# Optimization experiments

Hardware: AMD Instinct MI355X
Metric: run time of the kernel (lower is better)

Reference implementation:

```python
import jax, jax.numpy as jnp
import numpy as np

B, T, H, C, R = 8, 8192, 128, 128, 128  # batch, points, hidden, c_dim, plane reso
EPS = 1e-3  # 10e-4 in original
PLANE_COLS = ((0, 2), (0, 1), (1, 2))  # xz, xy, yz


def _normalize_coordinate(p, cols):
    # normalize_coordinate with padding=0.0: p in [-0.5,0.5] -> [0,1), clipped
    xy = p[..., jnp.array(cols)] / (1.0 + 0.0 + EPS) + 0.5
    return jnp.clip(xy, 0.0, 1.0 - EPS)


def _coordinate2index(xy):
    g = jnp.floor(xy * R).astype(jnp.int32)  # [B,T,2]
    return g[..., 0] + R * g[..., 1]  # [B,T]


def _resblock(x, w0, b0, w1, b1, ws):
    # ResnetBlockFC: fc_1(relu(fc_0(relu(x)))) + shortcut(x)
    net = jax.nn.relu(x) @ w0 + b0
    dx = jax.nn.relu(net) @ w1 + b1
    return x @ ws + dx


def _pool_local(c, idx_list):
    # c: [B,T,F]; scatter_max into R*R bins per plane, gather back, sum over planes
    def one(cb, ib):  # cb [T,F], ib [T]
        out = jnp.full((R * R, cb.shape[-1]), -jnp.inf, cb.dtype).at[ib].max(cb)
        out = jnp.where(jnp.isinf(out), jnp.zeros_like(out), out)  # empty bins -> 0
        return out[ib]  # gather-broadcast back to points
    pooled = jnp.zeros_like(c)
    for idx in idx_list:
        pooled = pooled + jax.vmap(one)(c, idx)
    return pooled


def _plane_features(cfeat, idx):
    # scatter_mean of [B,T,C] into [B, C, R, R]
    def one(cb, ib):  # cb [T,C], ib [T]
        sums = jnp.zeros((R * R, cb.shape[-1]), cb.dtype).at[ib].add(cb)
        cnt = jnp.zeros((R * R,), cb.dtype).at[ib].add(1.0)
        return sums / jnp.clip(cnt, 1.0, None)[:, None]
    m = jax.vmap(one)(cfeat, idx)  # [B, R*R, C]
    return m.transpose(0, 2, 1).reshape(cfeat.shape[0], cfeat.shape[-1], R, R)


def _forward(p, p2, wp, bp, wp2, bp2,
             blk_w0, blk_b0, blk_w1, blk_b1, blk_ws,
             blkc_w0, blkc_b0, blkc_w1, blkc_b1, blkc_ws,
             fc_c_w, fc_c_b, fc_cc_w, fc_cc_b):
    idx_list = [_coordinate2index(_normalize_coordinate(p, cols)) for cols in PLANE_COLS]

    # feat_pos (PointNetPlusPlusAttnFusion) surrogate: per-point projections + additive fusion
    net = p @ wp + bp                  # [B,T,2H] geometry stream
    net_corr = net + (p2 @ wp2 + bp2)  # [B,T,2H] fused articulation stream

    net = _resblock(net, blk_w0[0], blk_b0[0], blk_w1[0], blk_b1[0], blk_ws[0])
    for i in range(1, blk_w0.shape[0]):
        pooled = _pool_local(net, idx_list)
        net = _resblock(jnp.concatenate([net, pooled], axis=-1),
                        blk_w0[i], blk_b0[i], blk_w1[i], blk_b1[i], blk_ws[i])
    c = net @ fc_c_w + fc_c_b  # [B,T,C]

    net_corr = _resblock(net_corr, blkc_w0[0], blkc_b0[0], blkc_w1[0], blkc_b1[0], blkc_ws[0])
    for i in range(1, blkc_w0.shape[0]):
        pooled = _pool_local(net_corr, idx_list)
        net_corr = _resblock(jnp.concatenate([net_corr, pooled], axis=-1),
                             blkc_w0[i], blkc_b0[i], blkc_w1[i], blkc_b1[i], blkc_ws[i])
    c_corr = net_corr @ fc_cc_w + fc_cc_b  # [B,T,C]

    planes = [_plane_features(c, idx) for idx in idx_list]
    planes += [_plane_features(c_corr, idx) for idx in idx_list]
    # order: geo_xz, geo_xy, geo_yz, corr_xz, corr_xy, corr_yz
    return jnp.stack(planes)  # [6, B, C, R, R]


def setup_inputs() -> dict:
    key = jax.random.key(0)
    ks = jax.random.split(key, 24)
    s = 0.05
    def n(i, shape):
        return jax.random.normal(ks[i], shape, jnp.float32) * s
    NB = 5
    return {
        "p": jax.random.uniform(ks[0], (B, T, 3), jnp.float32, -0.5, 0.5),
        "p2": jax.random.uniform(ks[1], (B, T, 3), jnp.float32, -0.5, 0.5),
        "wp": n(2, (3, 2 * H)), "bp": jnp.zeros((2 * H,), jnp.float32),
        "wp2": n(3, (3, 2 * H)), "bp2": jnp.zeros((2 * H,), jnp.float32),
        "blk_w0": n(4, (NB, 2 * H, H)), "blk_b0": jnp.zeros((NB, H), jnp.float32),
        "blk_w1": n(5, (NB, H, H)), "blk_b1": jnp.zeros((NB, H), jnp.float32),
        "blk_ws": n(6, (NB, 2 * H, H)),
        "blkc_w0": n(7, (NB, 2 * H, H)), "blkc_b0": jnp.zeros((NB, H), jnp.float32),
        "blkc_w1": n(8, (NB, H, H)), "blkc_b1": jnp.zeros((NB, H), jnp.float32),
        "blkc_ws": n(9, (NB, 2 * H, H)),
        "fc_c_w": n(10, (H, C)), "fc_c_b": jnp.zeros((C,), jnp.float32),
        "fc_cc_w": n(11, (H, C)), "fc_cc_b": jnp.zeros((C,), jnp.float32),
    }


def reference(p, p2, wp, bp, wp2, bp2,
              blk_w0, blk_b0, blk_w1, blk_b1, blk_ws,
              blkc_w0, blkc_b0, blkc_w1, blkc_b1, blkc_ws,
              fc_c_w, fc_c_b, fc_cc_w, fc_cc_b):
    return _forward(p, p2, wp, bp, wp2, bp2,
                    blk_w0, blk_b0, blk_w1, blk_b1, blk_ws,
                    blkc_w0, blkc_b0, blkc_w1, blkc_b1, blkc_ws,
                    fc_c_w, fc_c_b, fc_cc_w, fc_cc_b)
```

## Files before the change

### kernel.cpp

```cpp
#include <hip/hip_runtime.h>
#include <cstdint>
#include <cstddef>

#define Bn 8
#define Tn 8192
#define BT (Bn*Tn)
#define Hn 128
#define RRn 16384

typedef unsigned short u16;
typedef __attribute__((ext_vector_type(8))) short s8v;
typedef __attribute__((ext_vector_type(4))) float f4v;

#define SSTR ((size_t)BT*128)

__device__ __forceinline__ u16 f2bf(float f) {
  unsigned u = __float_as_uint(f);
  unsigned r = (u + 0x7FFF + ((u >> 16) & 1)) >> 16;
  return (u16)r;
}
__device__ __forceinline__ unsigned pack2(float a, float b) {
  return (unsigned)f2bf(a) | ((unsigned)f2bf(b) << 16);
}

__device__ __forceinline__ s8v relu8(s8v a) {
  union { s8v s; unsigned u[4]; } x; x.s = a;
#pragma unroll
  for (int k = 0; k < 4; ++k) {
    unsigned m = ((x.u[k] & 0x80008000u) >> 15) * 0xFFFFu;
    x.u[k] &= ~m;
  }
  return x.s;
}

__device__ __forceinline__ void upk(unsigned u, float& lo, float& hi) {
  lo = __uint_as_float(u << 16);
  hi = __uint_as_float(u & 0xFFFF0000u);
}

__global__ void k_idx(const float* __restrict__ p, int* __restrict__ idx,
                      int* __restrict__ cnt32) {
  int i = blockIdx.x*256 + threadIdx.x;
  if (i >= BT) return;
  int b = i >> 13;
  float v0 = p[i*3+0], v1 = p[i*3+1], v2 = p[i*3+2];
  float v[3] = {v0, v1, v2};
  const int A0[3] = {0,0,1};
  const int A1[3] = {2,1,2};
#pragma unroll
  for (int pl = 0; pl < 3; ++pl) {
    float a = v[A0[pl]] / 1.001f + 0.5f;
    float bq = v[A1[pl]] / 1.001f + 0.5f;
    a = fminf(fmaxf(a, 0.0f), 0.999f);
    bq = fminf(fmaxf(bq, 0.0f), 0.999f);
    int ga = (int)floorf(a * 128.0f);
    int gb = (int)floorf(bq * 128.0f);
    int bin = ga + 128*gb;
    idx[pl*BT + i] = bin;
    atomicAdd(&cnt32[(pl*Bn + b)*RRn + bin], 1);
  }
}

__global__ void k_scan(const int* __restrict__ cnt32, int* __restrict__ starts,
                       int* __restrict__ cursor) {
  int seg = blockIdx.x;
  const int* c = cnt32 + seg*RRn;
  int* st = starts + seg*RRn;
  int* cu = cursor + seg*RRn;
  int t = threadIdx.x;
  __shared__ int part[256];
  int base = t*64;
  int sum = 0;
#pragma unroll 8
  for (int j = 0; j < 64; ++j) sum += c[base+j];
  part[t] = sum; __syncthreads();
  for (int ofs = 1; ofs < 256; ofs <<= 1) {
    int v = (t >= ofs) ? part[t-ofs] : 0;
    __syncthreads();
    part[t] += v;
    __syncthreads();
  }
  int run = (t ? part[t-1] : 0) + seg*Tn;
#pragma unroll 8
  for (int j = 0; j < 64; ++j) { st[base+j] = run; cu[base+j] = run; run += c[base+j]; }
}

__global__ void k_fill(const int* __restrict__ idx, int* __restrict__ cursor,
                       int* __restrict__ sorted) {
  int g = blockIdx.x*256 + threadIdx.x;
  if (g >= 3*BT) return;
  int pl = g >> 16, i = g & (BT-1);
  int b = i >> 13;
  int pos = atomicAdd(&cursor[(pl*Bn + b)*RRn + idx[g]], 1);
  sorted[pos] = i;
}

__global__ void k_prep(const float* __restrict__ bw0, const float* __restrict__ bw1,
                       const float* __restrict__ bws, const float* __restrict__ cw0,
                       const float* __restrict__ cw1, const float* __restrict__ cws,
                       const float* __restrict__ fcw, const float* __restrict__ fccw,
                       u16* __restrict__ arena) {
  int c = blockIdx.x;
  int s = c / 26, r = c % 26;
  const float* base;
  if (r < 10)      base = (s ? cw0 : bw0) + (size_t)(r >> 1)*32768 + (size_t)(r & 1)*16384;
  else if (r < 15) base = (s ? cw1 : bw1) + (size_t)(r - 10)*16384;
  else if (r < 25) base = (s ? cws : bws) + (size_t)((r - 15) >> 1)*32768 + (size_t)((r - 15) & 1)*16384;
  else             base = s ? fccw : fcw;
  __shared__ u16 ld[128*130];
#pragma unroll 4
  for (int it = 0; it < 64; ++it) {
    int lin = it*256 + threadIdx.x;
    int k = lin >> 7, n = lin & 127;
    ld[k*130 + n] = f2bf(base[lin]);
  }
  __syncthreads();
  u16* dst = arena + (size_t)c*16384;
#pragma unroll 4
  for (int it = 0; it < 64; ++it) {
    int lin = it*256 + threadIdx.x;
    int n = lin >> 7, k = lin & 127;
    dst[lin] = ld[k*130 + n];
  }
}

template<int MODE>
__global__ __launch_bounds__(512, 2) void k_rb(
    const u16* __restrict__ xAb, const u16* __restrict__ xBb,
    const float* __restrict__ p, const float* __restrict__ p2,
    const float* __restrict__ wp, const float* __restrict__ bp,
    const float* __restrict__ wp2, const float* __restrict__ bp2,
    const u16* __restrict__ arena,
    int cw00, int cw01, int cws0, int cws1, int cw1c, int cfcw,
    const float* __restrict__ b0g, const float* __restrict__ b0c,
    const float* __restrict__ b1g, const float* __restrict__ b1c,
    const float* __restrict__ fcbg, const float* __restrict__ fcbc,
    u16* __restrict__ outb)
{
  const int y = blockIdx.y;
  const u16* ar = arena + (size_t)y*26*16384;
  const u16* w00 = ar + (size_t)cw00*16384;
  const u16* w01 = ar + (size_t)cw01*16384;
  const u16* ws0 = ar + (size_t)cws0*16384;
  const u16* ws1 = ar + (size_t)cws1*16384;
  const u16* w1c = ar + (size_t)cw1c*16384;
  const u16* fcw = ar + (size_t)cfcw*16384;
  const float* b0 = y ? b0c : b0g;
  const float* b1 = y ? b1c : b1g;
  const float* fcb = y ? fcbc : fcbg;
  const u16* xA = xAb + (size_t)y*SSTR;
  const u16* xB = xBb + (size_t)y*SSTR;
  u16* outp = outb + (size_t)y*SSTR;

  __shared__ u16 xs [256*72];
  __shared__ u16 w0s[128*72];
  __shared__ u16 wss[128*72];
  __shared__ u16 hid[256*136];
  const int tid = threadIdx.x;
  const size_t row0 = (size_t)blockIdx.x * 256;
  const int l = tid & 63, w = tid >> 6;
  const int lm = l & 15, lg = l >> 4;
  const int trow = tid >> 1, th = tid & 1;
  const int wn = tid >> 2, wq = tid & 3;

  f4v acc_h[2][8], acc_s[2][8];
#pragma unroll
  for (int mi = 0; mi < 2; ++mi)
#pragma unroll
    for (int j = 0; j < 8; ++j) { acc_h[mi][j] = (f4v){0,0,0,0}; acc_s[mi][j] = (f4v){0,0,0,0}; }

  float pa0=0.f, pa1=0.f, pa2=0.f, pq0=0.f, pq1=0.f, pq2=0.f;
  if (MODE == 1) {
    int rr = (int)row0 + trow;
    pa0 = p[rr*3+0]; pa1 = p[rr*3+1]; pa2 = p[rr*3+2];
    if (y) { pq0 = p2[rr*3+0]; pq1 = p2[rr*3+1]; pq2 = p2[rr*3+2]; }
  }

  uint4 px0, px1, px2, px3, pwa, pwb, psa, psb;
  if (MODE != 1) {
    const uint4* s = (const uint4*)(xA + (row0 + trow)*128 + th*32);
    px0 = s[0]; px1 = s[1]; px2 = s[2]; px3 = s[3];
  }
  {
    const uint4* sw = (const uint4*)(w00 + wn*128 + wq*16);
    pwa = sw[0]; pwb = sw[1];
    const uint4* ss = (const uint4*)(ws0 + wn*128 + wq*16);
    psa = ss[0]; psb = ss[1];
  }

#pragma unroll 1
  for (int kc = 0; kc < 4; ++kc) {
    if (MODE == 1) {
      const int c0 = kc*64 + th*32;
      unsigned t16[16];
#pragma unroll
      for (int q = 0; q < 8; ++q) {
        int c = c0 + q*4;
        float4 w0v = *(const float4*)(wp + c);
        float4 w1v = *(const float4*)(wp + 256 + c);
        float4 w2v = *(const float4*)(wp + 512 + c);
        float4 bbv = *(const float4*)(bp + c);
        float v0 = pa0*w0v.x + pa1*w1v.x + pa2*w2v.x + bbv.x;
        float v1 = pa0*w0v.y + pa1*w1v.y + pa2*w2v.y + bbv.y;
        float v2 = pa0*w0v.z + pa1*w1v.z + pa2*w2v.z + bbv.z;
        float v3 = pa0*w0v.w + pa1*w1v.w + pa2*w2v.w + bbv.w;
        if (y) {
          float4 u0 = *(const float4*)(wp2 + c);
          float4 u1 = *(const float4*)(wp2 + 256 + c);
          float4 u2 = *(const float4*)(wp2 + 512 + c);
          float4 b2 = *(const float4*)(bp2 + c);
          v0 += pq0*u0.x + pq1*u1.x + pq2*u2.x + b2.x;
          v1 += pq0*u0.y + pq1*u1.y + pq2*u2.y + b2.y;
          v2 += pq0*u0.z + pq1*u1.z + pq2*u2.z + b2.z;
          v3 += pq0*u0.w + pq1*u1.w + pq2*u2.w + b2.w;
        }
        t16[q*2]   = pack2(v0, v1);
        t16[q*2+1] = pack2(v2, v3);
      }
      uint4* d = (uint4*)(xs + trow*72 + th*32);
      d[0] = make_uint4(t16[0], t16[1], t16[2], t16[3]);
      d[1] = make_uint4(t16[4], t16[5], t16[6], t16[7]);
      d[2] = make_uint4(t16[8], t16[9], t16[10], t16[11]);
      d[3] = make_uint4(t16[12], t16[13], t16[14], t16[15]);
    } else {
      uint4* d = (uint4*)(xs + trow*72 + th*32);
      d[0] = px0; d[1] = px1; d[2] = px2; d[3] = px3;
    }
    { uint4* d = (uint4*)(w0s + wn*72 + wq*16); d[0] = pwa; d[1] = pwb; }
    { uint4* d = (uint4*)(wss + wn*72 + wq*16); d[0] = psa; d[1] = psb; }
    __syncthreads();
    if (kc < 3) {
      const int kn = kc + 1;
      const int k0n = (kn & 1) * 64;
      if (MODE != 1) {
        const u16* xsrcn = (kn < 2) ? xA : xB;
        const uint4* s = (const uint4*)(xsrcn + (row0 + trow)*128 + k0n + th*32);
        px0 = s[0]; px1 = s[1]; px2 = s[2]; px3 = s[3];
      }
      const u16* w0srcn = (kn < 2) ? w00 : w01;
      const u16* wssrcn = (kn < 2) ? ws0 : ws1;
      const uint4* sw = (const uint4*)(w0srcn + wn*128 + k0n + wq*16);
      pwa = sw[0]; pwb = sw[1];
      const uint4* ss = (const uint4*)(wssrcn + wn*128 + k0n + wq*16);
      psa = ss[0]; psb = ss[1];
    }
#pragma unroll
    for (int kk = 0; kk < 2; ++kk) {
      const int ko = lg*8 + kk*32;
      s8v a0 = *(const s8v*)(xs + (w*32 + lm)*72 + ko);
      s8v a1 = *(const s8v*)(xs + (w*32 + 16 + lm)*72 + ko);
      s8v a0r = relu8(a0), a1r = relu8(a1);
#pragma unroll
      for (int nj = 0; nj < 8; ++nj) {
        s8v bh = *(const s8v*)(w0s + (nj*16 + lm)*72 + ko);
        acc_h[0][nj] = __builtin_amdgcn_mfma_f32_16x16x32_bf16(a0r, bh, acc_h[0][nj], 0, 0, 0);
        acc_h[1][nj] = __builtin_amdgcn_mfma_f32_16x16x32_bf16(a1r, bh, acc_h[1][nj], 0, 0, 0);
      }
#pragma unroll
      for (int nj = 0; nj < 8; ++nj) {
        s8v bs = *(const s8v*)(wss + (nj*16 + lm)*72 + ko);
        acc_s[0][nj] = __builtin_amdgcn_mfma_f32_16x16x32_bf16(a0, bs, acc_s[0][nj], 0, 0, 0);
        acc_s[1][nj] = __builtin_amdgcn_mfma_f32_16x16x32_bf16(a1, bs, acc_s[1][nj], 0, 0, 0);
      }
    }
    __syncthreads();
  }
  {
    const uint4* s1 = (const uint4*)(w1c + wn*128 + wq*16);
    uint4 aa = s1[0], bb2 = s1[1];
    const uint4* s2 = (const uint4*)(w1c + wn*128 + 64 + wq*16);
    uint4 cc = s2[0], dd = s2[1];
    { uint4* d = (uint4*)(w0s + wn*72 + wq*16); d[0] = aa; d[1] = bb2; }
    { uint4* d = (uint4*)(wss + wn*72 + wq*16); d[0] = cc; d[1] = dd; }
#pragma unroll
    for (int mi = 0; mi < 2; ++mi)
#pragma unroll
      for (int nj = 0; nj < 8; ++nj) {
        const int col = nj*16 + lm;
        const float bv = b0[col];
#pragma unroll
        for (int r = 0; r < 4; ++r) {
          int row = w*32 + mi*16 + lg*4 + r;
          hid[row*136 + col] = f2bf(fmaxf(acc_h[mi][nj][r] + bv, 0.0f));
        }
      }
  }
  __syncthreads();
#pragma unroll
  for (int kk = 0; kk < 4; ++kk) {
    const int koA = lg*8 + kk*32;
    const int koB = lg*8 + (kk & 1)*32;
    const u16* pb = (kk < 2) ? w0s : wss;
    s8v a0 = *(const s8v*)(hid + (w*32 + lm)*136 + koA);
    s8v a1 = *(const s8v*)(hid + (w*32 + 16 + lm)*136 + koA);
#pragma unroll
    for (int nj = 0; nj < 8; ++nj) {
      s8v bb = *(const s8v*)(pb + (nj*16 + lm)*72 + koB);
      acc_s[0][nj] = __builtin_amdgcn_mfma_f32_16x16x32_bf16(a0, bb, acc_s[0][nj], 0, 0, 0);
      acc_s[1][nj] = __builtin_amdgcn_mfma_f32_16x16x32_bf16(a1, bb, acc_s[1][nj], 0, 0, 0);
    }
  }
  if (MODE != 2) {
#pragma unroll
    for (int mi = 0; mi < 2; ++mi)
#pragma unroll
      for (int nj = 0; nj < 8; ++nj) {
        const int col = nj*16 + lm;
        const float bv = b1[col];
#pragma unroll
        for (int r = 0; r < 4; ++r) {
          int row = w*32 + mi*16 + lg*4 + r;
          outp[(row0 + row)*128 + col] = f2bf(acc_s[mi][nj][r] + bv);
        }
      }
  } else {
    __syncthreads();
    {
      const uint4* s1 = (const uint4*)(fcw + wn*128 + wq*16);
      uint4 aa = s1[0], bb2 = s1[1];
      const uint4* s2 = (const uint4*)(fcw + wn*128 + 64 + wq*16);
      uint4 cc = s2[0], dd = s2[1];
      { uint4* d = (uint4*)(w0s + wn*72 + wq*16); d[0] = aa; d[1] = bb2; }
      { uint4* d = (uint4*)(wss + wn*72 + wq*16); d[0] = cc; d[1] = dd; }
#pragma unroll
      for (int mi = 0; mi < 2; ++mi)
#pragma unroll
        for (int nj = 0; nj < 8; ++nj) {
          const int col = nj*16 + lm;
          const float bv = b1[col];
#pragma unroll
          for (int r = 0; r < 4; ++r) {
            int row = w*32 + mi*16 + lg*4 + r;
            hid[row*136 + col] = f2bf(acc_s[mi][nj][r] + bv);
          }
        }
    }
    __syncthreads();
    f4v accf[2][8];
#pragma unroll
    for (int mi = 0; mi < 2; ++mi)
#pragma unroll
      for (int j = 0; j < 8; ++j) accf[mi][j] = (f4v){0,0,0,0};
#pragma unroll
    for (int kk = 0; kk < 4; ++kk) {
      const int koA = lg*8 + kk*32;
      const int koB = lg*8 + (kk & 1)*32;
      const u16* pb = (kk < 2) ? w0s : wss;
      s8v a0 = *(const s8v*)(hid + (w*32 + lm)*136 + koA);
      s8v a1 = *(const s8v*)(hid + (w*32 + 16 + lm)*136 + koA);
#pragma unroll
      for (int nj = 0; nj < 8; ++nj) {
        s8v bb = *(const s8v*)(pb + (nj*16 + lm)*72 + koB);
        accf[0][nj] = __builtin_amdgcn_mfma_f32_16x16x32_bf16(a0, bb, accf[0][nj], 0, 0, 0);
        accf[1][nj] = __builtin_amdgcn_mfma_f32_16x16x32_bf16(a1, bb, accf[1][nj], 0, 0, 0);
      }
    }
#pragma unroll
    for (int mi = 0; mi < 2; ++mi)
#pragma unroll
      for (int nj = 0; nj < 8; ++nj) {
        const int col = nj*16 + lm;
        const float bv = fcb[col];
#pragma unroll
        for (int r = 0; r < 4; ++r) {
          int row = w*32 + mi*16 + lg*4 + r;
          outp[(row0 + row)*128 + col] = f2bf(accf[mi][nj][r] + bv);
        }
      }
  }
}

__global__ void k_pool(const int* __restrict__ idx, const int* __restrict__ starts,
                       const int* __restrict__ cnt32, const int* __restrict__ sorted,
                       const u16* __restrict__ netb, u16* __restrict__ pooledb) {
  const u16* net = netb + (size_t)blockIdx.y*SSTR;
  u16* pooled = pooledb + (size_t)blockIdx.y*SSTR;
  int g = blockIdx.x*256 + threadIdx.x;
  int sl = g & 15;
  int i = g >> 4;
  if (i >= BT) return;
  int b = i >> 13;
  float acc[8];
#pragma unroll
  for (int k = 0; k < 8; ++k) acc[k] = 0.0f;
#pragma unroll
  for (int pl = 0; pl < 3; ++pl) {
    int seg = (pl*Bn + b)*RRn + idx[pl*BT + i];
    int s = starts[seg];
    int e = s + cnt32[seg];
    float mx[8];
#pragma unroll
    for (int k = 0; k < 8; ++k) mx[k] = -3.0e38f;
    for (int j = s; j < e; ++j) {
      int jj = sorted[j];
      uint4 v = *(const uint4*)(net + (size_t)jj*128 + sl*8);
      float lo, hi;
      upk(v.x, lo, hi); mx[0] = fmaxf(mx[0], lo); mx[1] = fmaxf(mx[1], hi);
      upk(v.y, lo, hi); mx[2] = fmaxf(mx[2], lo); mx[3] = fmaxf(mx[3], hi);
      upk(v.z, lo, hi); mx[4] = fmaxf(mx[4], lo); mx[5] = fmaxf(mx[5], hi);
      upk(v.w, lo, hi); mx[6] = fmaxf(mx[6], lo); mx[7] = fmaxf(mx[7], hi);
    }
#pragma unroll
    for (int k = 0; k < 8; ++k) acc[k] += mx[k];
  }
  union { uint4 v; unsigned u[4]; } o;
#pragma unroll
  for (int k = 0; k < 4; ++k)
    o.u[k] = (unsigned)f2bf(acc[2*k]) | ((unsigned)f2bf(acc[2*k+1]) << 16);
  *(uint4*)(pooled + (size_t)i*128 + sl*8) = o.v;
}

__global__ __launch_bounds__(256) void k_mean(
    const int* __restrict__ starts, const int* __restrict__ cnt32,
    const int* __restrict__ sorted, const u16* __restrict__ cbufb,
    float* __restrict__ out) {
  int W = blockIdx.x*4 + (threadIdx.x >> 6);
  int lane = threadIdx.x & 63;
  int grp = W & 255;
  int b = (W >> 8) & 7;
  int plq = W >> 11;
  int ss = plq / 3, pl = plq - 3*ss;
  int bin = grp*64 + lane;
  int seg = (pl*Bn + b)*RRn + bin;
  int c = cnt32[seg];
  int s0 = starts[seg];
  float inv = (c > 0) ? 1.0f/(float)c : 0.0f;
  const u16* cb = cbufb + (size_t)ss*SSTR;
  size_t obase = ((size_t)(plq*Bn + b)*Hn)*RRn + bin;
#pragma unroll 1
  for (int half = 0; half < 2; ++half) {
    float sum[64];
#pragma unroll
    for (int k = 0; k < 64; ++k) sum[k] = 0.f;
    for (int j = 0; j < c; ++j) {
      int jj = sorted[s0 + j];
      const uint4* r = (const uint4*)(cb + (size_t)jj*128 + half*64);
#pragma unroll
      for (int k = 0; k < 8; ++k) {
        uint4 q = r[k];
        float lo, hi;
        upk(q.x, lo, hi); sum[k*8+0] += lo; sum[k*8+1] += hi;
        upk(q.y, lo, hi); sum[k*8+2] += lo; sum[k*8+3] += hi;
        upk(q.z, lo, hi); sum[k*8+4] += lo; sum[k*8+5] += hi;
        upk(q.w, lo, hi); sum[k*8+6] += lo; sum[k*8+7] += hi;
      }
    }
#pragma unroll
    for (int k = 0; k < 64; ++k)
      out[obase + (size_t)(half*64 + k)*RRn] = sum[k]*inv;
  }
}

extern "C" void kernel_launch(void* const* d_in, const int* in_sizes, int n_in,
                              void* d_out_v, int out_size, void* d_ws, size_t ws_size,
                              hipStream_t stream) {
  const float* p    = (const float*)d_in[0];
  const float* p2   = (const float*)d_in[1];
  const float* wp   = (const float*)d_in[2];
  const float* bp   = (const float*)d_in[3];
  const float* wp2  = (const float*)d_in[4];
  const float* bp2  = (const float*)d_in[5];
  const float* bw0  = (const float*)d_in[6];
  const float* bb0  = (const float*)d_in[7];
  const float* bw1  = (const float*)d_in[8];
  const float* bb1  = (const float*)d_in[9];
  const float* bws  = (const float*)d_in[10];
  const float* cw0  = (const float*)d_in[11];
  const float* cb0  = (const float*)d_in[12];
  const float* cw1  = (const float*)d_in[13];
  const float* cb1  = (const float*)d_in[14];
  const float* cws  = (const float*)d_in[15];
  const float* fcw  = (const float*)d_in[16];
  const float* fcb  = (const float*)d_in[17];
  const float* fccw = (const float*)d_in[18];
  const float* fccb = (const float*)d_in[19];
  float* out = (float*)d_out_v;

  size_t off = 0;
  auto alloc = [&](size_t bytes) -> char* {
    char* r = (char*)d_ws + off;
    off += (bytes + 255) & ~(size_t)255;
    return r;
  };
  int* idx    = (int*)alloc((size_t)3*BT*4);
  int* cnt32  = (int*)alloc((size_t)3*Bn*RRn*4);
  int* starts = (int*)alloc((size_t)3*Bn*RRn*4);
  int* cursor = (int*)alloc((size_t)3*Bn*RRn*4);
  int* sorted = (int*)alloc((size_t)3*BT*4);
  u16* arena  = (u16*)alloc((size_t)52*16384*2);
  u16* buf0   = (u16*)alloc(2*SSTR*2);
  u16* buf1   = (u16*)alloc(2*SSTR*2);
  u16* bufP   = (u16*)alloc(2*SSTR*2);
  u16* cbuf   = (u16*)alloc(2*SSTR*2);
  if (off > ws_size) return;

  hipMemsetAsync(cnt32, 0, (size_t)3*Bn*RRn*4, stream);
  k_prep<<<52, 256, 0, stream>>>(bw0, bw1, bws, cw0, cw1, cws, fcw, fccw, arena);
  k_idx <<<BT/256, 256, 0, stream>>>(p, idx, cnt32);
  k_scan<<<24, 256, 0, stream>>>(cnt32, starts, cursor);
  k_fill<<<(3*BT)/256, 256, 0, stream>>>(idx, cursor, sorted);

  k_rb<1><<<dim3(BT/256, 2), 512, 0, stream>>>(
      nullptr, nullptr, p, p2, wp, bp, wp2, bp2,
      arena, 0, 1, 15, 16, 10, 25,
      bb0, cb0, bb1, cb1, nullptr, nullptr, buf1);
  u16* net = buf1; u16* other = buf0;
  for (int blk = 1; blk < 4; ++blk) {
    k_pool<<<dim3((BT*16)/256, 2), 256, 0, stream>>>(idx, starts, cnt32, sorted, net, bufP);
    k_rb<0><<<dim3(BT/256, 2), 512, 0, stream>>>(
        net, bufP, nullptr, nullptr, nullptr, nullptr, nullptr, nullptr,
        arena, 2*blk, 2*blk+1, 15+2*blk, 16+2*blk, 10+blk, 25,
        bb0 + blk*128, cb0 + blk*128, bb1 + blk*128, cb1 + blk*128,
        nullptr, nullptr, other);
    u16* t = net; net = other; other = t;
  }
  k_pool<<<dim3((BT*16)/256, 2), 256, 0, stream>>>(idx, starts, cnt32, sorted, net, bufP);
  k_rb<2><<<dim3(BT/256, 2), 512, 0, stream>>>(
      net, bufP, nullptr, nullptr, nullptr, nullptr, nullptr, nullptr,
      arena, 8, 9, 23, 24, 14, 25,
      bb0 + 4*128, cb0 + 4*128, bb1 + 4*128, cb1 + 4*128, fcb, fccb, cbuf);

  k_mean<<<3072, 256, 0, stream>>>(starts, cnt32, sorted, cbuf, out);
}
```

Measured before the change: 526.3 us.

## Fuse local max-pool gather into resblock kernel prologue

Removes the separate k_pool kernel and the pooled bf16 buffer. Each resblock kernel now gathers the per-plane max-pooled features for its 256 rows directly into shared memory (the hid buffer) and feeds the second half of the K dimension from there. This saves a write and re-read of the pooled tensor and four kernel launches per forward. The cost is a serial, latency-bound gather loop at the start of the MFMA kernel, with two threads per row instead of sixteen, which runs with lower parallelism at 2 blocks per CU.

```diff
diff --git a/kernel.cpp b/kernel.cpp
--- a/kernel.cpp
+++ b/kernel.cpp
@@ -126,10 +126,12 @@
 
 template<int MODE>
 __global__ __launch_bounds__(512, 2) void k_rb(
-    const u16* __restrict__ xAb, const u16* __restrict__ xBb,
+    const u16* __restrict__ xAb,
     const float* __restrict__ p, const float* __restrict__ p2,
     const float* __restrict__ wp, const float* __restrict__ bp,
     const float* __restrict__ wp2, const float* __restrict__ bp2,
+    const int* __restrict__ idxg, const int* __restrict__ startsg,
+    const int* __restrict__ cnt32g, const int* __restrict__ sortedg,
     const u16* __restrict__ arena,
     int cw00, int cw01, int cws0, int cws1, int cw1c, int cfcw,
     const float* __restrict__ b0g, const float* __restrict__ b0c,
@@ -149,7 +151,6 @@
   const float* b1 = y ? b1c : b1g;
   const float* fcb = y ? fcbc : fcbg;
   const u16* xA = xAb + (size_t)y*SSTR;
-  const u16* xB = xBb + (size_t)y*SSTR;
   u16* outp = outb + (size_t)y*SSTR;
 
   __shared__ u16 xs [256*72];
@@ -186,6 +187,55 @@
     pwa = sw[0]; pwb = sw[1];
     const uint4* ss = (const uint4*)(ws0 + wn*128 + wq*16);
     psa = ss[0]; psb = ss[1];
+  }
+
+  if (MODE != 1) {
+    const int gi = (int)row0 + trow;
+    const int bb = gi >> 13;
+    int segS[3], segC[3];
+#pragma unroll
+    for (int pl = 0; pl < 3; ++pl) {
+      int s_ = (pl*Bn + bb)*RRn + idxg[pl*BT + gi];
+      segS[pl] = startsg[s_]; segC[pl] = cnt32g[s_];
+    }
+#pragma unroll 1
+    for (int sub = 0; sub < 4; ++sub) {
+      const int ch0 = th*64 + sub*16;
+      float acc[16];
+#pragma unroll
+      for (int k = 0; k < 16; ++k) acc[k] = 0.f;
+#pragma unroll
+      for (int pl = 0; pl < 3; ++pl) {
+        int s0 = segS[pl], c = segC[pl];
+        float mx[16];
+#pragma unroll
+        for (int k = 0; k < 16; ++k) mx[k] = -3.0e38f;
+        for (int j = 0; j < c; ++j) {
+          int jj = sortedg[s0 + j];
+          const uint4* r = (const uint4*)(xA + (size_t)jj*128 + ch0);
+          uint4 q0 = r[0], q1 = r[1];
+          float lo, hi;
+          upk(q0.x, lo, hi); mx[0]=fmaxf(mx[0],lo);   mx[1]=fmaxf(mx[1],hi);
+          upk(q0.y, lo, hi); mx[2]=fmaxf(mx[2],lo);   mx[3]=fmaxf(mx[3],hi);
+          upk(q0.z, lo, hi); mx[4]=fmaxf(mx[4],lo);   mx[5]=fmaxf(mx[5],hi);
+          upk(q0.w, lo, hi); mx[6]=fmaxf(mx[6],lo);   mx[7]=fmaxf(mx[7],hi);
+          upk(q1.x, lo, hi); mx[8]=fmaxf(mx[8],lo);   mx[9]=fmaxf(mx[9],hi);
+          upk(q1.y, lo, hi); mx[10]=fmaxf(mx[10],lo); mx[11]=fmaxf(mx[11],hi);
+          upk(q1.z, lo, hi); mx[12]=fmaxf(mx[12],lo); mx[13]=fmaxf(mx[13],hi);
+          upk(q1.w, lo, hi); mx[14]=fmaxf(mx[14],lo); mx[15]=fmaxf(mx[15],hi);
+        }
+#pragma unroll
+        for (int k = 0; k < 16; ++k) acc[k] += mx[k];
+      }
+      union { uint4 v; unsigned u[4]; } o0, o1;
+#pragma unroll
+      for (int k = 0; k < 4; ++k) {
+        o0.u[k] = pack2(acc[2*k],     acc[2*k+1]);
+        o1.u[k] = pack2(acc[8 + 2*k], acc[8 + 2*k+1]);
+      }
+      *(uint4*)(hid + trow*136 + ch0)     = o0.v;
+      *(uint4*)(hid + trow*136 + ch0 + 8) = o1.v;
+    }
   }
 
 #pragma unroll 1
@@ -222,7 +272,7 @@
       d[1] = make_uint4(t16[4], t16[5], t16[6], t16[7]);
       d[2] = make_uint4(t16[8], t16[9], t16[10], t16[11]);
       d[3] = make_uint4(t16[12], t16[13], t16[14], t16[15]);
-    } else {
+    } else if (kc < 2) {
       uint4* d = (uint4*)(xs + trow*72 + th*32);
       d[0] = px0; d[1] = px1; d[2] = px2; d[3] = px3;
     }
@@ -232,9 +282,8 @@
     if (kc < 3) {
       const int kn = kc + 1;
       const int k0n = (kn & 1) * 64;
-      if (MODE != 1) {
-        const u16* xsrcn = (kn < 2) ? xA : xB;
-        const uint4* s = (const uint4*)(xsrcn + (row0 + trow)*128 + k0n + th*32);
+      if (MODE != 1 && kn == 1) {
+        const uint4* s = (const uint4*)(xA + (row0 + trow)*128 + 64 + th*32);
         px0 = s[0]; px1 = s[1]; px2 = s[2]; px3 = s[3];
       }
       const u16* w0srcn = (kn < 2) ? w00 : w01;
@@ -246,19 +295,26 @@
     }
 #pragma unroll
     for (int kk = 0; kk < 2; ++kk) {
-      const int ko = lg*8 + kk*32;
-      s8v a0 = *(const s8v*)(xs + (w*32 + lm)*72 + ko);
-      s8v a1 = *(const s8v*)(xs + (w*32 + 16 + lm)*72 + ko);
+      s8v a0, a1;
+      if (MODE == 1 || kc < 2) {
+        const int ko = lg*8 + kk*32;
+        a0 = *(const s8v*)(xs + (w*32 + lm)*72 + ko);
+        a1 = *(const s8v*)(xs + (w*32 + 16 + lm)*72 + ko);
+      } else {
+        const int ko = (kc & 1)*64 + lg*8 + kk*32;
+        a0 = *(const s8v*)(hid + (w*32 + lm)*136 + ko);
+        a1 = *(const s8v*)(hid + (w*32 + 16 + lm)*136 + ko);
+      }
       s8v a0r = relu8(a0), a1r = relu8(a1);
 #pragma unroll
       for (int nj = 0; nj < 8; ++nj) {
-        s8v bh = *(const s8v*)(w0s + (nj*16 + lm)*72 + ko);
+        s8v bh = *(const s8v*)(w0s + (nj*16 + lm)*72 + lg*8 + kk*32);
         acc_h[0][nj] = __builtin_amdgcn_mfma_f32_16x16x32_bf16(a0r, bh, acc_h[0][nj], 0, 0, 0);
         acc_h[1][nj] = __builtin_amdgcn_mfma_f32_16x16x32_bf16(a1r, bh, acc_h[1][nj], 0, 0, 0);
       }
 #pragma unroll
       for (int nj = 0; nj < 8; ++nj) {
-        s8v bs = *(const s8v*)(wss + (nj*16 + lm)*72 + ko);
+        s8v bs = *(const s8v*)(wss + (nj*16 + lm)*72 + lg*8 + kk*32);
         acc_s[0][nj] = __builtin_amdgcn_mfma_f32_16x16x32_bf16(a0, bs, acc_s[0][nj], 0, 0, 0);
         acc_s[1][nj] = __builtin_amdgcn_mfma_f32_16x16x32_bf16(a1, bs, acc_s[1][nj], 0, 0, 0);
       }
@@ -368,46 +424,6 @@
         }
       }
   }
-}
-
-__global__ void k_pool(const int* __restrict__ idx, const int* __restrict__ starts,
-                       const int* __restrict__ cnt32, const int* __restrict__ sorted,
-                       const u16* __restrict__ netb, u16* __restrict__ pooledb) {
-  const u16* net = netb + (size_t)blockIdx.y*SSTR;
-  u16* pooled = pooledb + (size_t)blockIdx.y*SSTR;
-  int g = blockIdx.x*256 + threadIdx.x;
-  int sl = g & 15;
-  int i = g >> 4;
-  if (i >= BT) return;
-  int b = i >> 13;
-  float acc[8];
-#pragma unroll
-  for (int k = 0; k < 8; ++k) acc[k] = 0.0f;
-#pragma unroll
-  for (int pl = 0; pl < 3; ++pl) {
-    int seg = (pl*Bn + b)*RRn + idx[pl*BT + i];
-    int s = starts[seg];
-    int e = s + cnt32[seg];
-    float mx[8];
-#pragma unroll
-    for (int k = 0; k < 8; ++k) mx[k] = -3.0e38f;
-    for (int j = s; j < e; ++j) {
-      int jj = sorted[j];
-      uint4 v = *(const uint4*)(net + (size_t)jj*128 + sl*8);
-      float lo, hi;
-      upk(v.x, lo, hi); mx[0] = fmaxf(mx[0], lo); mx[1] = fmaxf(mx[1], hi);
-      upk(v.y, lo, hi); mx[2] = fmaxf(mx[2], lo); mx[3] = fmaxf(mx[3], hi);
-      upk(v.z, lo, hi); mx[4] = fmaxf(mx[4], lo); mx[5] = fmaxf(mx[5], hi);
-      upk(v.w, lo, hi); mx[6] = fmaxf(mx[6], lo); mx[7] = fmaxf(mx[7], hi);
-    }
-#pragma unroll
-    for (int k = 0; k < 8; ++k) acc[k] += mx[k];
-  }
-  union { uint4 v; unsigned u[4]; } o;
-#pragma unroll
-  for (int k = 0; k < 4; ++k)
-    o.u[k] = (unsigned)f2bf(acc[2*k]) | ((unsigned)f2bf(acc[2*k+1]) << 16);
-  *(uint4*)(pooled + (size_t)i*128 + sl*8) = o.v;
 }
 
 __global__ __launch_bounds__(256) void k_mean(
@@ -490,7 +506,6 @@
   u16* arena  = (u16*)alloc((size_t)52*16384*2);
   u16* buf0   = (u16*)alloc(2*SSTR*2);
   u16* buf1   = (u16*)alloc(2*SSTR*2);
-  u16* bufP   = (u16*)alloc(2*SSTR*2);
   u16* cbuf   = (u16*)alloc(2*SSTR*2);
   if (off > ws_size) return;
 
@@ -501,22 +516,23 @@
   k_fill<<<(3*BT)/256, 256, 0, stream>>>(idx, cursor, sorted);
 
   k_rb<1><<<dim3(BT/256, 2), 512, 0, stream>>>(
-      nullptr, nullptr, p, p2, wp, bp, wp2, bp2,
+      nullptr, p, p2, wp, bp, wp2, bp2,
+      nullptr, nullptr, nullptr, nullptr,
       arena, 0, 1, 15, 16, 10, 25,
       bb0, cb0, bb1, cb1, nullptr, nullptr, buf1);
   u16* net = buf1; u16* other = buf0;
   for (int blk = 1; blk < 4; ++blk) {
-    k_pool<<<dim3((BT*16)/256, 2), 256, 0, stream>>>(idx, starts, cnt32, sorted, net, bufP);
     k_rb<0><<<dim3(BT/256, 2), 512, 0, stream>>>(
-        net, bufP, nullptr, nullptr, nullptr, nullptr, nullptr, nullptr,
+        net, nullptr, nullptr, nullptr, nullptr, nullptr, nullptr,
+        idx, starts, cnt32, sorted,
         arena, 2*blk, 2*blk+1, 15+2*blk, 16+2*blk, 10+blk, 25,
         bb0 + blk*128, cb0 + blk*128, bb1 + blk*128, cb1 + blk*128,
         nullptr, nullptr, other);
     u16* t = net; net = other; other = t;
   }
-  k_pool<<<dim3((BT*16)/256, 2), 256, 0, stream>>>(idx, starts, cnt32, sorted, net, bufP);
   k_rb<2><<<dim3(BT/256, 2), 512, 0, stream>>>(
-      net, bufP, nullptr, nullptr, nullptr, nullptr, nullptr, nullptr,
+      net, nullptr, nullptr, nullptr, nullptr, nullptr, nullptr,
+      idx, starts, cnt32, sorted,
       arena, 8, 9, 23, 24, 14, 25,
       bb0 + 4*128, cb0 + 4*128, bb1 + 4*128, cb1 + 4*128, fcb, fccb, cbuf);
 
```

Measured after the change: 672.6 us. +27.8%, slower.
